# Performance work log

Measured on AMD Instinct MI355X. Metric: run time of the kernel, lower is better.

## Reference

```python
import jax, jax.numpy as jnp
import numpy as np

B, S, H = 2, 2048, 4096
NH, NKV, D = 32, 8, 128          # query heads, kv heads, head_dim = H // NH
G = NH // NKV                    # GQA group size
THETA = 10000.0


def setup_inputs() -> dict:
    key = jax.random.key(0)
    k1, k2, k3 = jax.random.split(key, 3)
    hidden_states = jax.random.normal(k1, (B, S, H), dtype=jnp.float32)
    positions = jnp.tile(jnp.arange(S, dtype=jnp.int64 if jax.config.jax_enable_x64 else jnp.int32), (B, 1))
    w_qkv = jax.random.normal(k2, (H, (NH + 2 * NKV) * D), dtype=jnp.float32) * 0.02
    w_o = jax.random.normal(k3, (NH * D, H), dtype=jnp.float32) * 0.02
    return {"hidden_states": hidden_states, "positions": positions, "w_qkv": w_qkv, "w_o": w_o}


def _rope_interleaved(x, positions, theta):
    # is_neox_style=False: rotate interleaved (even, odd) pairs. x: [B,S,Hh,D]
    d = x.shape[-1]
    inv_freq = 1.0 / (theta ** (jnp.arange(0, d, 2, dtype=jnp.float32) / d))  # [D/2]
    freqs = positions.astype(jnp.float32)[..., None] * inv_freq               # [B,S,D/2]
    cos = jnp.cos(freqs)[:, :, None, :]
    sin = jnp.sin(freqs)[:, :, None, :]
    x1 = x[..., 0::2]
    x2 = x[..., 1::2]
    o1 = x1 * cos - x2 * sin
    o2 = x2 * cos + x1 * sin
    return jnp.stack([o1, o2], axis=-1).reshape(x.shape)


def reference(hidden_states, positions, w_qkv, w_o):
    qkv = hidden_states @ w_qkv                                   # [B,S,(NH+2*NKV)*D]
    q, k, v = jnp.split(qkv, [NH * D, NH * D + NKV * D], axis=-1)
    q = q.reshape(B, S, NH, D)
    k = k.reshape(B, S, NKV, D)
    v = v.reshape(B, S, NKV, D)
    q = _rope_interleaved(q, positions, THETA)
    k = _rope_interleaved(k, positions, THETA)
    # GQA: group query heads per kv head instead of repeating k/v
    qg = q.reshape(B, S, NKV, G, D)
    scores = jnp.einsum('bqhgd,bkhd->bhgqk', qg, k) * (D ** -0.5)  # [B,NKV,G,S,S]
    causal = jnp.tril(jnp.ones((S, S), dtype=bool))
    scores = jnp.where(causal, scores, jnp.finfo(scores.dtype).min)
    probs = jax.nn.softmax(scores, axis=-1)
    out = jnp.einsum('bhgqk,bkhd->bqhgd', probs, v).reshape(B, S, NH * D)
    return out @ w_o                                              # [B,S,H]
```

## Files before the change

### kernel.cpp

```cpp
#include <hip/hip_runtime.h>
#include <cmath>

#define B_    2
#define S_    2048
#define H_    4096
#define NH_   32
#define NKV_  8
#define D_    128
#define QKV_N 6144
#define MTOK  4096

typedef __attribute__((ext_vector_type(8))) short bf16x8;
typedef __attribute__((ext_vector_type(4))) float f32x4;
typedef __attribute__((ext_vector_type(4))) unsigned short us4;

#define GLL16(gp, lp)                                                         \
  __builtin_amdgcn_global_load_lds(                                           \
      (const __attribute__((address_space(1))) void*)(gp),                    \
      (__attribute__((address_space(3))) void*)(lp), 16, 0, 0)

__device__ __forceinline__ unsigned short f2bf(float f) {
  unsigned u = __float_as_uint(f);
  u += 0x7fff + ((u >> 16) & 1);
  return (unsigned short)(u >> 16);
}

__global__ __launch_bounds__(256) void cast_bf16_kernel(const float* __restrict__ in,
                                                        unsigned short* __restrict__ out,
                                                        int n4) {
  int i = blockIdx.x * blockDim.x + threadIdx.x;
  if (i >= n4) return;
  float4 v = ((const float4*)in)[i];
  us4 o;
  o.x = f2bf(v.x); o.y = f2bf(v.y); o.z = f2bf(v.z); o.w = f2bf(v.w);
  ((us4*)out)[i] = o;
}

__global__ __launch_bounds__(256) void transpose_cast_kernel(const float* __restrict__ w,
                                                             unsigned short* __restrict__ wt,
                                                             int K, int N) {
  __shared__ float tile[32][33];
  const int k0 = blockIdx.y * 32, n0 = blockIdx.x * 32;
  const int tid = threadIdx.x;
  const int r = tid >> 3, c4 = (tid & 7) * 4;
  float4 v = *(const float4*)(w + (size_t)(k0 + r) * N + n0 + c4);
  tile[r][c4 + 0] = v.x; tile[r][c4 + 1] = v.y;
  tile[r][c4 + 2] = v.z; tile[r][c4 + 3] = v.w;
  __syncthreads();
  us4 o;
  o.x = f2bf(tile[c4 + 0][r]);
  o.y = f2bf(tile[c4 + 1][r]);
  o.z = f2bf(tile[c4 + 2][r]);
  o.w = f2bf(tile[c4 + 3][r]);
  *(us4*)(wt + (size_t)(n0 + r) * K + k0 + c4) = o;
}

__global__ __launch_bounds__(256) void gemm_bt_kernel(const unsigned short* __restrict__ A,
                                                      const unsigned short* __restrict__ Bt,
                                                      float* __restrict__ C,
                                                      int M, int N, int K) {
  __shared__ short As[128 * 32];
  __shared__ short Bs[128 * 32];
  const int tid = threadIdx.x;
  const int w = tid >> 6, lane = tid & 63;
  const int quad = lane >> 4, l16 = lane & 15;
  const int nx = (int)gridDim.x;
  const int nwg = nx * (int)gridDim.y;
  const int oid = (int)blockIdx.y * nx + (int)blockIdx.x;
  const int cpx = nwg >> 3;
  const int sid = (oid & 7) * cpx + (oid >> 3);
  const int bn = sid % nx, bm = sid / nx;
  const int mbase = (w & 1) * 64, nbase = (w >> 1) * 64;

  f32x4 acc[4][4] = {};

  const int srow = w * 32 + (lane >> 2);
  const int skoff = (lane & 3) * 8;
  const unsigned short* Ap = A + (size_t)(bm * 128 + srow) * K + skoff;
  const unsigned short* Bp = Bt + (size_t)(bn * 128 + srow) * K + skoff;

  for (int k0 = 0; k0 < K; k0 += 32) {
    __syncthreads();
#pragma unroll
    for (int i = 0; i < 2; ++i) {
      GLL16(Ap + (size_t)i * 16 * K + k0, As + (w * 32 + i * 16) * 32);
      GLL16(Bp + (size_t)i * 16 * K + k0, Bs + (w * 32 + i * 16) * 32);
    }
    __syncthreads();
    bf16x8 af[4], bfr[4];
#pragma unroll
    for (int mi = 0; mi < 4; ++mi)
      af[mi] = *(const bf16x8*)(As + (mbase + mi * 16 + l16) * 32 + quad * 8);
#pragma unroll
    for (int nj = 0; nj < 4; ++nj)
      bfr[nj] = *(const bf16x8*)(Bs + (nbase + nj * 16 + l16) * 32 + quad * 8);
#pragma unroll
    for (int mi = 0; mi < 4; ++mi)
#pragma unroll
      for (int nj = 0; nj < 4; ++nj)
        acc[mi][nj] = __builtin_amdgcn_mfma_f32_16x16x32_bf16(af[mi], bfr[nj], acc[mi][nj], 0, 0, 0);
  }

  float* Cp = C + (size_t)(bm * 128 + mbase + quad * 4) * N + bn * 128 + nbase + l16;
#pragma unroll
  for (int mi = 0; mi < 4; ++mi)
#pragma unroll
    for (int nj = 0; nj < 4; ++nj)
#pragma unroll
      for (int r = 0; r < 4; ++r)
        Cp[(size_t)(mi * 16 + r) * N + nj * 16] = acc[mi][nj][r];
}

__global__ __launch_bounds__(256) void rope_cast_kernel(const float* __restrict__ qkv,
                                                        const int* __restrict__ positions,
                                                        unsigned short* __restrict__ qkvb) {
  const int tok = blockIdx.y;
  const int p = blockIdx.x * 256 + threadIdx.x;
  const float2 x = *(const float2*)(qkv + (size_t)tok * QKV_N + 2 * p);
  float o1, o2;
  if (p < (NH_ + NKV_) * (D_ / 2)) {
    const int j = p & 63;
    const float inv = exp2f((float)(2 * j) * (-13.287712379549449f / 128.f));
    const float f = (float)positions[tok] * inv;
    float s, c;
    sincosf(f, &s, &c);
    o1 = x.x * c - x.y * s;
    o2 = x.y * c + x.x * s;
  } else {
    o1 = x.x; o2 = x.y;
  }
  unsigned r = (unsigned)f2bf(o1) | ((unsigned)f2bf(o2) << 16);
  *(unsigned*)(qkvb + (size_t)tok * QKV_N + 2 * p) = r;
}

__global__ __launch_bounds__(256) void vtrans_kernel(const unsigned short* __restrict__ qkvb,
                                                     unsigned short* __restrict__ vT) {
  __shared__ unsigned short t[32][33];
  const int s0 = blockIdx.x * 32;
  const int y0 = blockIdx.y * 32;
  const int b = y0 >> 10;
  const int col0 = (NH_ + NKV_) * D_ + (y0 & 1023);
  const int tid = threadIdx.x;
  const int r = tid >> 3, c4 = (tid & 7) * 4;
  us4 v = *(const us4*)(qkvb + (size_t)(b * S_ + s0 + r) * QKV_N + col0 + c4);
  t[r][c4 + 0] = v.x; t[r][c4 + 1] = v.y;
  t[r][c4 + 2] = v.z; t[r][c4 + 3] = v.w;
  __syncthreads();
  us4 o;
  o.x = t[c4 + 0][r]; o.y = t[c4 + 1][r];
  o.z = t[c4 + 2][r]; o.w = t[c4 + 3][r];
  *(us4*)(vT + (size_t)(y0 + r) * S_ + s0 + c4) = o;
}

__global__ __launch_bounds__(256) void attn_mfma_kernel(const unsigned short* __restrict__ qkvb,
                                                        const unsigned short* __restrict__ vT,
                                                        unsigned short* __restrict__ aoutb) {
  __shared__ short Ks[2][32 * 128];
  __shared__ short Vs[2][32 * 128];
  const int p = (int)blockIdx.x;
  const int o = ((p >> 3) & 63) + 64 * ((p & 7) + 8 * (p >> 9));
  const int qt = 15 - (o & 15);
  const int h = (o >> 4) & 31;
  const int b = o >> 9;
  const int kvh = h >> 2;
  const int tid = threadIdx.x;
  const int w = tid >> 6, lane = tid & 63;
  const int quad = lane >> 4, l16 = lane & 15;
  const int qbase = qt * 128 + w * 32;

  bf16x8 qf0[4], qf1[4];
  {
    const unsigned short* qp0 = qkvb + (size_t)(b * S_ + qbase + l16) * QKV_N + h * D_ + quad * 8;
    const unsigned short* qp1 = qp0 + (size_t)16 * QKV_N;
#pragma unroll
    for (int kk = 0; kk < 4; ++kk) {
      qf0[kk] = *(const bf16x8*)(qp0 + kk * 32);
      qf1[kk] = *(const bf16x8*)(qp1 + kk * 32);
    }
  }

  unsigned ks0, ks1, vs0, vs1;
  {
    int i0 = w * 64 + lane;
    int i1 = i0 + 256;
    int r0 = i0 >> 4, c0 = i0 & 15;
    int r1 = i1 >> 4, c1 = i1 & 15;
    int cs0 = (c0 & 8) | ((c0 ^ r0) & 7);
    int cs1 = (c1 & 8) | ((c1 ^ r1) & 7);
    ks0 = (unsigned)(b * S_ + r0) * QKV_N + NH_ * D_ + kvh * D_ + cs0 * 8;
    ks1 = (unsigned)(b * S_ + r1) * QKV_N + NH_ * D_ + kvh * D_ + cs1 * 8;
    int vr0 = i0 >> 2, vc0 = i0 & 3;
    int vr1 = i1 >> 2, vc1 = i1 & 3;
    int vcs0 = vc0 ^ ((vr0 & 3) ^ ((vr0 >> 2) & 3));
    int vcs1 = vc1 ^ ((vr1 & 3) ^ ((vr1 >> 2) & 3));
    vs0 = (unsigned)((b * NKV_ + kvh) * D_ + vr0) * S_ + vcs0 * 8;
    vs1 = (unsigned)((b * NKV_ + kvh) * D_ + vr1) * S_ + vcs1 * 8;
  }

#define STAGE_KV(bufi, kbv)                                                   \
  {                                                                           \
    const unsigned short* kgp_ = qkvb + (size_t)(kbv) * QKV_N;                \
    short* KsW_ = &Ks[bufi][w * 512];                                         \
    short* VsW_ = &Vs[bufi][w * 512];                                         \
    GLL16(kgp_ + ks0, KsW_);                                                  \
    GLL16(kgp_ + ks1, KsW_ + 2048);                                           \
    GLL16(vT + vs0 + (kbv), VsW_);                                            \
    GLL16(vT + vs1 + (kbv), VsW_ + 2048);                                     \
  }

  const int kbase = l16 * 128 + ((quad ^ (l16 & 3)) << 3);
  const int mh5 = ((l16 >> 2) & 1) << 5;
  const int swl = (l16 & 3) ^ ((l16 >> 2) & 3);
  const int vbase = l16 * 32 + ((quad ^ swl) << 3);

  float mreg[2] = {-1e30f, -1e30f};
  float lreg[2] = {0.f, 0.f};
  f32x4 oacc0[8] = {};
  f32x4 oacc1[8] = {};

  const int qmaxw = qbase + 31;
  const int ntiles = 4 * qt + 4;
  const float SCL = 0.08838834764831845f * 1.4426950408889634f;

  STAGE_KV(0, 0);
  for (int kt = 0; kt < ntiles; ++kt) {
    const int kb = kt * 32;
    const int cur = kt & 1;
    if (kt + 1 < ntiles) {
      STAGE_KV(cur ^ 1, kb + 32);
      asm volatile("s_waitcnt vmcnt(4)" ::: "memory");
    } else {
      asm volatile("s_waitcnt vmcnt(0)" ::: "memory");
    }
    __builtin_amdgcn_s_barrier();
    if (kb <= qmaxw) {
      const short* Kc = Ks[cur];
      const short* Vc = Vs[cur];
      f32x4 st00 = {}, st01 = {}, st10 = {}, st11 = {};
      __builtin_amdgcn_s_setprio(1);
#pragma unroll
      for (int kk = 0; kk < 4; ++kk) {
        const int ko = (kk << 5) ^ mh5;
        bf16x8 kf0 = *(const bf16x8*)(Kc + kbase + ko);
        bf16x8 kf1 = *(const bf16x8*)(Kc + kbase + 2048 + ko);
        st00 = __builtin_amdgcn_mfma_f32_16x16x32_bf16(kf0, qf0[kk], st00, 0, 0, 0);
        st01 = __builtin_amdgcn_mfma_f32_16x16x32_bf16(kf1, qf0[kk], st01, 0, 0, 0);
        st10 = __builtin_amdgcn_mfma_f32_16x16x32_bf16(kf0, qf1[kk], st10, 0, 0, 0);
        st11 = __builtin_amdgcn_mfma_f32_16x16x32_bf16(kf1, qf1[kk], st11, 0, 0, 0);
      }
      __builtin_amdgcn_s_setprio(0);
      bf16x8 pf[2];
      float al[2][4];
#pragma unroll
      for (int s = 0; s < 2; ++s) {
        const f32x4 a0 = s ? st10 : st00;
        const f32x4 a1 = s ? st11 : st01;
        float sc[8];
#pragma unroll
        for (int r = 0; r < 4; ++r) {
          sc[r] = a0[r] * SCL;
          sc[4 + r] = a1[r] * SCL;
        }
        const int qrow = qbase + s * 16 + l16;
        if (kb + 31 > qbase + s * 16) {
          const int kvb0 = kb + quad * 4;
#pragma unroll
          for (int r = 0; r < 4; ++r) {
            if (kvb0 + r > qrow) sc[r] = -1e30f;
            if (kvb0 + 16 + r > qrow) sc[4 + r] = -1e30f;
          }
        }
        float cmax = sc[0];
#pragma unroll
        for (int i = 1; i < 8; ++i) cmax = fmaxf(cmax, sc[i]);
        cmax = fmaxf(cmax, __shfl_xor(cmax, 16));
        cmax = fmaxf(cmax, __shfl_xor(cmax, 32));
        const float mo = mreg[s];
        const float mn = fmaxf(mo, cmax);
        const float alpha = exp2f(mo - mn);
        mreg[s] = mn;
        float pr[8];
        float ps = 0.f;
#pragma unroll
        for (int i = 0; i < 8; ++i) { pr[i] = exp2f(sc[i] - mn); ps += pr[i]; }
        lreg[s] = lreg[s] * alpha + ps;
        unsigned pw00 = (unsigned)f2bf(pr[0]) | ((unsigned)f2bf(pr[1]) << 16);
        unsigned pw01 = (unsigned)f2bf(pr[2]) | ((unsigned)f2bf(pr[3]) << 16);
        unsigned pw10 = (unsigned)f2bf(pr[4]) | ((unsigned)f2bf(pr[5]) << 16);
        unsigned pw11 = (unsigned)f2bf(pr[6]) | ((unsigned)f2bf(pr[7]) << 16);
        const int srcA = l16 + ((quad & 1) << 5);
        const int srcB = srcA + 16;
        unsigned g0 = __shfl(pw00, srcA), g1 = __shfl(pw01, srcA);
        unsigned g2 = __shfl(pw10, srcA), g3 = __shfl(pw11, srcA);
        unsigned h0 = __shfl(pw00, srcB), h1 = __shfl(pw01, srcB);
        unsigned h2 = __shfl(pw10, srcB), h3 = __shfl(pw11, srcB);
        const bool loq = quad < 2;
        union { unsigned u[4]; bf16x8 v; } pu;
        pu.u[0] = loq ? g0 : g2;
        pu.u[1] = loq ? g1 : g3;
        pu.u[2] = loq ? h0 : h2;
        pu.u[3] = loq ? h1 : h3;
        pf[s] = pu.v;
        const int abase = (lane & 48) | (quad << 2);
        al[s][0] = __shfl(alpha, abase);
        al[s][1] = __shfl(alpha, abase + 1);
        al[s][2] = __shfl(alpha, abase + 2);
        al[s][3] = __shfl(alpha, abase + 3);
      }
      __builtin_amdgcn_s_setprio(1);
#pragma unroll
      for (int n2 = 0; n2 < 8; ++n2) {
        bf16x8 vf = *(const bf16x8*)(Vc + vbase + n2 * 512);
        oacc0[n2][0] *= al[0][0]; oacc0[n2][1] *= al[0][1];
        oacc0[n2][2] *= al[0][2]; oacc0[n2][3] *= al[0][3];
        oacc0[n2] = __builtin_amdgcn_mfma_f32_16x16x32_bf16(pf[0], vf, oacc0[n2], 0, 0, 0);
        oacc1[n2][0] *= al[1][0]; oacc1[n2][1] *= al[1][1];
        oacc1[n2][2] *= al[1][2]; oacc1[n2][3] *= al[1][3];
        oacc1[n2] = __builtin_amdgcn_mfma_f32_16x16x32_bf16(pf[1], vf, oacc1[n2], 0, 0, 0);
      }
      __builtin_amdgcn_s_setprio(0);
    }
    __builtin_amdgcn_s_barrier();
  }

#define ATTN_EPI(sI, OA)                                                      \
  {                                                                           \
    float lsv = lreg[sI];                                                     \
    lsv += __shfl_xor(lsv, 16);                                               \
    lsv += __shfl_xor(lsv, 32);                                               \
    const float inv = 1.f / lsv;                                              \
    const int ab_ = (lane & 48) | (quad << 2);                                \
    const float i0 = __shfl(inv, ab_), i1 = __shfl(inv, ab_ + 1);             \
    const float i2 = __shfl(inv, ab_ + 2), i3 = __shfl(inv, ab_ + 3);         \
    unsigned short* op = aoutb +                                              \
        (size_t)(b * S_ + qbase + sI * 16 + quad * 4) * (NH_ * D_) +          \
        h * D_ + l16;                                                         \
    _Pragma("unroll")                                                         \
    for (int n2 = 0; n2 < 8; ++n2) {                                          \
      op[0 * (NH_ * D_) + n2 * 16] = f2bf(OA[n2][0] * i0);                    \
      op[1 * (NH_ * D_) + n2 * 16] = f2bf(OA[n2][1] * i1);                    \
      op[2 * (NH_ * D_) + n2 * 16] = f2bf(OA[n2][2] * i2);                    \
      op[3 * (NH_ * D_) + n2 * 16] = f2bf(OA[n2][3] * i3);                    \
    }                                                                         \
  }
  ATTN_EPI(0, oacc0);
  ATTN_EPI(1, oacc1);
#undef ATTN_EPI
#undef STAGE_KV
}

extern "C" void kernel_launch(void* const* d_in, const int* in_sizes, int n_in,
                              void* d_out, int out_size, void* d_ws, size_t ws_size,
                              hipStream_t stream) {
  const float* hs    = (const float*)d_in[0];
  const int*   pos   = (const int*)d_in[1];
  const float* w_qkv = (const float*)d_in[2];
  const float* w_o   = (const float*)d_in[3];
  float* out = (float*)d_out;

  char* wsp = (char*)d_ws;
  float* qkv           = (float*)wsp;
  unsigned short* qkvb = (unsigned short*)(wsp + (size_t)MTOK * QKV_N * 4);
  unsigned short* bufB = (unsigned short*)(wsp + (size_t)MTOK * QKV_N * 6);
  unsigned short* bufC = bufB + (size_t)MTOK * H_;
  unsigned short* vT   = bufC + (size_t)MTOK * QKV_N;

  cast_bf16_kernel<<<(MTOK * H_ / 4 + 255) / 256, 256, 0, stream>>>(hs, bufB, MTOK * H_ / 4);
  {
    dim3 g(QKV_N / 32, H_ / 32);
    transpose_cast_kernel<<<g, 256, 0, stream>>>(w_qkv, bufC, H_, QKV_N);
  }

  {
    dim3 g(QKV_N / 128, MTOK / 128);
    gemm_bt_kernel<<<g, 256, 0, stream>>>(bufB, bufC, qkv, MTOK, QKV_N, H_);
  }

  {
    dim3 g((QKV_N / 2) / 256, MTOK);
    rope_cast_kernel<<<g, 256, 0, stream>>>(qkv, pos, qkvb);
  }

  {
    dim3 g(S_ / 32, (B_ * NKV_ * D_) / 32);
    vtrans_kernel<<<g, 256, 0, stream>>>(qkvb, vT);
  }

  {
    dim3 ga((S_ / 128) * NH_ * B_);
    attn_mfma_kernel<<<ga, 256, 0, stream>>>(qkvb, vT, bufC);
  }

  {
    dim3 g(H_ / 32, H_ / 32);
    transpose_cast_kernel<<<g, 256, 0, stream>>>(w_o, bufB, H_, H_);
  }

  {
    dim3 g(H_ / 128, MTOK / 128);
    gemm_bt_kernel<<<g, 256, 0, stream>>>(bufC, bufB, out, MTOK, H_, NH_ * D_);
  }
}
```

Measured before the change: 1.092 ms.

## Use single-wave attention blocks loading K/V directly from global memory

```diff
diff --git a/kernel.cpp b/kernel.cpp
--- a/kernel.cpp
+++ b/kernel.cpp
@@ -152,21 +152,20 @@
   *(us4*)(vT + (size_t)(y0 + r) * S_ + s0 + c4) = o;
 }
 
-__global__ __launch_bounds__(256) void attn_mfma_kernel(const unsigned short* __restrict__ qkvb,
-                                                        const unsigned short* __restrict__ vT,
-                                                        unsigned short* __restrict__ aoutb) {
-  __shared__ short Ks[2][32 * 128];
-  __shared__ short Vs[2][32 * 128];
+__global__ __launch_bounds__(64) void attn_mfma_kernel(const unsigned short* __restrict__ qkvb,
+                                                       const unsigned short* __restrict__ vT,
+                                                       unsigned short* __restrict__ aoutb) {
   const int p = (int)blockIdx.x;
-  const int o = ((p >> 3) & 63) + 64 * ((p & 7) + 8 * (p >> 9));
-  const int qt = 15 - (o & 15);
-  const int h = (o >> 4) & 31;
-  const int b = o >> 9;
-  const int kvh = h >> 2;
-  const int tid = threadIdx.x;
-  const int w = tid >> 6, lane = tid & 63;
+  const int xcd = p & 7;
+  const int o = p >> 3;
+  const int qt = 63 - (o >> 3);
+  const int hl = (o >> 1) & 3;
+  const int b = o & 1;
+  const int h = xcd * 4 + hl;
+  const int kvh = xcd;
+  const int lane = (int)threadIdx.x & 63;
   const int quad = lane >> 4, l16 = lane & 15;
-  const int qbase = qt * 128 + w * 32;
+  const int qbase = qt * 32;
 
   bf16x8 qf0[4], qf1[4];
   {
@@ -179,148 +178,116 @@
     }
   }
 
-  unsigned ks0, ks1, vs0, vs1;
-  {
-    int i0 = w * 64 + lane;
-    int i1 = i0 + 256;
-    int r0 = i0 >> 4, c0 = i0 & 15;
-    int r1 = i1 >> 4, c1 = i1 & 15;
-    int cs0 = (c0 & 8) | ((c0 ^ r0) & 7);
-    int cs1 = (c1 & 8) | ((c1 ^ r1) & 7);
-    ks0 = (unsigned)(b * S_ + r0) * QKV_N + NH_ * D_ + kvh * D_ + cs0 * 8;
-    ks1 = (unsigned)(b * S_ + r1) * QKV_N + NH_ * D_ + kvh * D_ + cs1 * 8;
-    int vr0 = i0 >> 2, vc0 = i0 & 3;
-    int vr1 = i1 >> 2, vc1 = i1 & 3;
-    int vcs0 = vc0 ^ ((vr0 & 3) ^ ((vr0 >> 2) & 3));
-    int vcs1 = vc1 ^ ((vr1 & 3) ^ ((vr1 >> 2) & 3));
-    vs0 = (unsigned)((b * NKV_ + kvh) * D_ + vr0) * S_ + vcs0 * 8;
-    vs1 = (unsigned)((b * NKV_ + kvh) * D_ + vr1) * S_ + vcs1 * 8;
-  }
-
-#define STAGE_KV(bufi, kbv)                                                   \
-  {                                                                           \
-    const unsigned short* kgp_ = qkvb + (size_t)(kbv) * QKV_N;                \
-    short* KsW_ = &Ks[bufi][w * 512];                                         \
-    short* VsW_ = &Vs[bufi][w * 512];                                         \
-    GLL16(kgp_ + ks0, KsW_);                                                  \
-    GLL16(kgp_ + ks1, KsW_ + 2048);                                           \
-    GLL16(vT + vs0 + (kbv), VsW_);                                            \
-    GLL16(vT + vs1 + (kbv), VsW_ + 2048);                                     \
-  }
-
-  const int kbase = l16 * 128 + ((quad ^ (l16 & 3)) << 3);
-  const int mh5 = ((l16 >> 2) & 1) << 5;
-  const int swl = (l16 & 3) ^ ((l16 >> 2) & 3);
-  const int vbase = l16 * 32 + ((quad ^ swl) << 3);
+  const unsigned short* kp = qkvb + (size_t)(b * S_ + l16) * QKV_N + NH_ * D_ + kvh * D_ + quad * 8;
+  const unsigned short* vp = vT + (size_t)((b * NKV_ + kvh) * D_ + l16) * S_ + quad * 8;
 
   float mreg[2] = {-1e30f, -1e30f};
   float lreg[2] = {0.f, 0.f};
   f32x4 oacc0[8] = {};
   f32x4 oacc1[8] = {};
 
-  const int qmaxw = qbase + 31;
-  const int ntiles = 4 * qt + 4;
   const float SCL = 0.08838834764831845f * 1.4426950408889634f;
 
-  STAGE_KV(0, 0);
-  for (int kt = 0; kt < ntiles; ++kt) {
+  for (int kt = 0; kt <= qt; ++kt) {
     const int kb = kt * 32;
-    const int cur = kt & 1;
-    if (kt + 1 < ntiles) {
-      STAGE_KV(cur ^ 1, kb + 32);
-      asm volatile("s_waitcnt vmcnt(4)" ::: "memory");
-    } else {
-      asm volatile("s_waitcnt vmcnt(0)" ::: "memory");
-    }
-    __builtin_amdgcn_s_barrier();
-    if (kb <= qmaxw) {
-      const short* Kc = Ks[cur];
-      const short* Vc = Vs[cur];
-      f32x4 st00 = {}, st01 = {}, st10 = {}, st11 = {};
-      __builtin_amdgcn_s_setprio(1);
-#pragma unroll
-      for (int kk = 0; kk < 4; ++kk) {
-        const int ko = (kk << 5) ^ mh5;
-        bf16x8 kf0 = *(const bf16x8*)(Kc + kbase + ko);
-        bf16x8 kf1 = *(const bf16x8*)(Kc + kbase + 2048 + ko);
-        st00 = __builtin_amdgcn_mfma_f32_16x16x32_bf16(kf0, qf0[kk], st00, 0, 0, 0);
-        st01 = __builtin_amdgcn_mfma_f32_16x16x32_bf16(kf1, qf0[kk], st01, 0, 0, 0);
-        st10 = __builtin_amdgcn_mfma_f32_16x16x32_bf16(kf0, qf1[kk], st10, 0, 0, 0);
-        st11 = __builtin_amdgcn_mfma_f32_16x16x32_bf16(kf1, qf1[kk], st11, 0, 0, 0);
+    const unsigned short* kpt = kp + (size_t)kb * QKV_N;
+    bf16x8 kf0[4], kf1[4];
+#pragma unroll
+    for (int kk = 0; kk < 4; ++kk) {
+      kf0[kk] = *(const bf16x8*)(kpt + kk * 32);
+      kf1[kk] = *(const bf16x8*)(kpt + (size_t)16 * QKV_N + kk * 32);
+    }
+    bf16x8 vf[8];
+#pragma unroll
+    for (int n2 = 0; n2 < 8; ++n2)
+      vf[n2] = *(const bf16x8*)(vp + (size_t)(n2 * 16) * S_ + kb);
+
+    f32x4 st00 = {}, st01 = {}, st10 = {}, st11 = {};
+    __builtin_amdgcn_s_setprio(1);
+#pragma unroll
+    for (int kk = 0; kk < 4; ++kk) {
+      st00 = __builtin_amdgcn_mfma_f32_16x16x32_bf16(kf0[kk], qf0[kk], st00, 0, 0, 0);
+      st01 = __builtin_amdgcn_mfma_f32_16x16x32_bf16(kf1[kk], qf0[kk], st01, 0, 0, 0);
+      st10 = __builtin_amdgcn_mfma_f32_16x16x32_bf16(kf0[kk], qf1[kk], st10, 0, 0, 0);
+      st11 = __builtin_amdgcn_mfma_f32_16x16x32_bf16(kf1[kk], qf1[kk], st11, 0, 0, 0);
+    }
+    __builtin_amdgcn_s_setprio(0);
+
+    bf16x8 pf[2];
+#pragma unroll
+    for (int s = 0; s < 2; ++s) {
+      const f32x4 a0 = s ? st10 : st00;
+      const f32x4 a1 = s ? st11 : st01;
+      float sc[8];
+#pragma unroll
+      for (int r = 0; r < 4; ++r) {
+        sc[r] = a0[r] * SCL;
+        sc[4 + r] = a1[r] * SCL;
       }
-      __builtin_amdgcn_s_setprio(0);
-      bf16x8 pf[2];
-      float al[2][4];
-#pragma unroll
-      for (int s = 0; s < 2; ++s) {
-        const f32x4 a0 = s ? st10 : st00;
-        const f32x4 a1 = s ? st11 : st01;
-        float sc[8];
+      const int qrow = qbase + s * 16 + l16;
+      if (kt == qt) {
+        const int kvb0 = kb + quad * 4;
 #pragma unroll
         for (int r = 0; r < 4; ++r) {
-          sc[r] = a0[r] * SCL;
-          sc[4 + r] = a1[r] * SCL;
+          if (kvb0 + r > qrow) sc[r] = -1e30f;
+          if (kvb0 + 16 + r > qrow) sc[4 + r] = -1e30f;
         }
-        const int qrow = qbase + s * 16 + l16;
-        if (kb + 31 > qbase + s * 16) {
-          const int kvb0 = kb + quad * 4;
-#pragma unroll
-          for (int r = 0; r < 4; ++r) {
-            if (kvb0 + r > qrow) sc[r] = -1e30f;
-            if (kvb0 + 16 + r > qrow) sc[4 + r] = -1e30f;
-          }
-        }
-        float cmax = sc[0];
-#pragma unroll
-        for (int i = 1; i < 8; ++i) cmax = fmaxf(cmax, sc[i]);
-        cmax = fmaxf(cmax, __shfl_xor(cmax, 16));
+      }
+      float pmax = sc[0];
+#pragma unroll
+      for (int i = 1; i < 8; ++i) pmax = fmaxf(pmax, sc[i]);
+      const float mo = mreg[s];
+      if (!__all(pmax - mo <= 8.f)) {
+        float cmax = fmaxf(pmax, __shfl_xor(pmax, 16));
         cmax = fmaxf(cmax, __shfl_xor(cmax, 32));
-        const float mo = mreg[s];
         const float mn = fmaxf(mo, cmax);
         const float alpha = exp2f(mo - mn);
         mreg[s] = mn;
-        float pr[8];
-        float ps = 0.f;
-#pragma unroll
-        for (int i = 0; i < 8; ++i) { pr[i] = exp2f(sc[i] - mn); ps += pr[i]; }
-        lreg[s] = lreg[s] * alpha + ps;
-        unsigned pw00 = (unsigned)f2bf(pr[0]) | ((unsigned)f2bf(pr[1]) << 16);
-        unsigned pw01 = (unsigned)f2bf(pr[2]) | ((unsigned)f2bf(pr[3]) << 16);
-        unsigned pw10 = (unsigned)f2bf(pr[4]) | ((unsigned)f2bf(pr[5]) << 16);
-        unsigned pw11 = (unsigned)f2bf(pr[6]) | ((unsigned)f2bf(pr[7]) << 16);
-        const int srcA = l16 + ((quad & 1) << 5);
-        const int srcB = srcA + 16;
-        unsigned g0 = __shfl(pw00, srcA), g1 = __shfl(pw01, srcA);
-        unsigned g2 = __shfl(pw10, srcA), g3 = __shfl(pw11, srcA);
-        unsigned h0 = __shfl(pw00, srcB), h1 = __shfl(pw01, srcB);
-        unsigned h2 = __shfl(pw10, srcB), h3 = __shfl(pw11, srcB);
-        const bool loq = quad < 2;
-        union { unsigned u[4]; bf16x8 v; } pu;
-        pu.u[0] = loq ? g0 : g2;
-        pu.u[1] = loq ? g1 : g3;
-        pu.u[2] = loq ? h0 : h2;
-        pu.u[3] = loq ? h1 : h3;
-        pf[s] = pu.v;
+        lreg[s] *= alpha;
         const int abase = (lane & 48) | (quad << 2);
-        al[s][0] = __shfl(alpha, abase);
-        al[s][1] = __shfl(alpha, abase + 1);
-        al[s][2] = __shfl(alpha, abase + 2);
-        al[s][3] = __shfl(alpha, abase + 3);
+        const float al0 = __shfl(alpha, abase);
+        const float al1 = __shfl(alpha, abase + 1);
+        const float al2 = __shfl(alpha, abase + 2);
+        const float al3 = __shfl(alpha, abase + 3);
+        f32x4* OA = s ? oacc1 : oacc0;
+#pragma unroll
+        for (int n2 = 0; n2 < 8; ++n2) {
+          OA[n2][0] *= al0; OA[n2][1] *= al1;
+          OA[n2][2] *= al2; OA[n2][3] *= al3;
+        }
       }
-      __builtin_amdgcn_s_setprio(1);
-#pragma unroll
-      for (int n2 = 0; n2 < 8; ++n2) {
-        bf16x8 vf = *(const bf16x8*)(Vc + vbase + n2 * 512);
-        oacc0[n2][0] *= al[0][0]; oacc0[n2][1] *= al[0][1];
-        oacc0[n2][2] *= al[0][2]; oacc0[n2][3] *= al[0][3];
-        oacc0[n2] = __builtin_amdgcn_mfma_f32_16x16x32_bf16(pf[0], vf, oacc0[n2], 0, 0, 0);
-        oacc1[n2][0] *= al[1][0]; oacc1[n2][1] *= al[1][1];
-        oacc1[n2][2] *= al[1][2]; oacc1[n2][3] *= al[1][3];
-        oacc1[n2] = __builtin_amdgcn_mfma_f32_16x16x32_bf16(pf[1], vf, oacc1[n2], 0, 0, 0);
-      }
-      __builtin_amdgcn_s_setprio(0);
-    }
-    __builtin_amdgcn_s_barrier();
+      const float mn2 = mreg[s];
+      float pr[8];
+      float ps = 0.f;
+#pragma unroll
+      for (int i = 0; i < 8; ++i) { pr[i] = exp2f(sc[i] - mn2); ps += pr[i]; }
+      lreg[s] += ps;
+      unsigned pw00 = (unsigned)f2bf(pr[0]) | ((unsigned)f2bf(pr[1]) << 16);
+      unsigned pw01 = (unsigned)f2bf(pr[2]) | ((unsigned)f2bf(pr[3]) << 16);
+      unsigned pw10 = (unsigned)f2bf(pr[4]) | ((unsigned)f2bf(pr[5]) << 16);
+      unsigned pw11 = (unsigned)f2bf(pr[6]) | ((unsigned)f2bf(pr[7]) << 16);
+      const int srcA = l16 + ((quad & 1) << 5);
+      const int srcB = srcA + 16;
+      unsigned g0 = __shfl(pw00, srcA), g1 = __shfl(pw01, srcA);
+      unsigned g2 = __shfl(pw10, srcA), g3 = __shfl(pw11, srcA);
+      unsigned h0 = __shfl(pw00, srcB), h1 = __shfl(pw01, srcB);
+      unsigned h2 = __shfl(pw10, srcB), h3 = __shfl(pw11, srcB);
+      const bool loq = quad < 2;
+      union { unsigned u[4]; bf16x8 v; } pu;
+      pu.u[0] = loq ? g0 : g2;
+      pu.u[1] = loq ? g1 : g3;
+      pu.u[2] = loq ? h0 : h2;
+      pu.u[3] = loq ? h1 : h3;
+      pf[s] = pu.v;
+    }
+
+    __builtin_amdgcn_s_setprio(1);
+#pragma unroll
+    for (int n2 = 0; n2 < 8; ++n2) {
+      oacc0[n2] = __builtin_amdgcn_mfma_f32_16x16x32_bf16(pf[0], vf[n2], oacc0[n2], 0, 0, 0);
+      oacc1[n2] = __builtin_amdgcn_mfma_f32_16x16x32_bf16(pf[1], vf[n2], oacc1[n2], 0, 0, 0);
+    }
+    __builtin_amdgcn_s_setprio(0);
   }
 
 #define ATTN_EPI(sI, OA)                                                      \
@@ -346,7 +313,6 @@
   ATTN_EPI(0, oacc0);
   ATTN_EPI(1, oacc1);
 #undef ATTN_EPI
-#undef STAGE_KV
 }
 
 extern "C" void kernel_launch(void* const* d_in, const int* in_sizes, int n_in,
@@ -386,10 +352,7 @@
     vtrans_kernel<<<g, 256, 0, stream>>>(qkvb, vT);
   }
 
-  {
-    dim3 ga((S_ / 128) * NH_ * B_);
-    attn_mfma_kernel<<<ga, 256, 0, stream>>>(qkvb, vT, bufC);
-  }
+  attn_mfma_kernel<<<(S_ / 32) * NH_ * B_, 64, 0, stream>>>(qkvb, vT, bufC);
 
   {
     dim3 g(H_ / 32, H_ / 32);
```

Measured after the change: 999.1 us. 8.5% less time.
